# Kernel optimization log

Measured on AMD Instinct MI355X. Metric: run time of the kernel, lower is better.

## Reference

```python
import jax, jax.numpy as jnp
import numpy as np

D_MODEL = 512
D_STATE = 16
D_CONV = 4
EXPAND = 2
D_INNER = EXPAND * D_MODEL          # 1024
DT_RANK = (D_MODEL + 15) // 16      # 32
B, L = 32, 2048
EPS = 1e-12


def _ln(x, g, b):
    mu = jnp.mean(x, axis=-1, keepdims=True)
    var = jnp.mean(jnp.square(x - mu), axis=-1, keepdims=True)
    return (x - mu) * jax.lax.rsqrt(var + EPS) * g + b


def setup_inputs() -> dict:
    key = jax.random.key(0)
    ks = jax.random.split(key, 12)
    s = lambda fan: 1.0 / np.sqrt(fan)
    inp = {
        "input_tensor": jax.random.normal(ks[0], (B, L, D_MODEL), jnp.float32),
        # Mamba params
        "in_proj_w": jax.random.normal(ks[1], (2 * D_INNER, D_MODEL), jnp.float32) * s(D_MODEL),
        "conv_w": jax.random.normal(ks[2], (D_INNER, D_CONV), jnp.float32) * s(D_CONV),
        "conv_b": jnp.zeros((D_INNER,), jnp.float32),
        "x_proj_w": jax.random.normal(ks[3], (DT_RANK + 2 * D_STATE, D_INNER), jnp.float32) * s(D_INNER),
        "dt_proj_w": jax.random.normal(ks[4], (D_INNER, DT_RANK), jnp.float32) * s(DT_RANK),
        "dt_proj_b": jnp.full((D_INNER,), -4.0, jnp.float32),  # softplus(-4) ~ small dt
        "A_log": jnp.log(jnp.broadcast_to(jnp.arange(1, D_STATE + 1, dtype=jnp.float32), (D_INNER, D_STATE))),
        "D": jnp.ones((D_INNER,), jnp.float32),
        "out_proj_w": jax.random.normal(ks[5], (D_MODEL, D_INNER), jnp.float32) * s(D_INNER),
        # block params
        "ln1_g": jnp.ones((D_MODEL,), jnp.float32),
        "ln1_b": jnp.zeros((D_MODEL,), jnp.float32),
        "w1_w": jax.random.normal(ks[6], (4 * D_MODEL, D_MODEL), jnp.float32) * s(D_MODEL),
        "w1_b": jnp.zeros((4 * D_MODEL,), jnp.float32),
        "w2_w": jax.random.normal(ks[7], (D_MODEL, 4 * D_MODEL), jnp.float32) * s(4 * D_MODEL),
        "w2_b": jnp.zeros((D_MODEL,), jnp.float32),
        "ln2_g": jnp.ones((D_MODEL,), jnp.float32),
        "ln2_b": jnp.zeros((D_MODEL,), jnp.float32),
    }
    return inp


def _mamba(x, in_proj_w, conv_w, conv_b, x_proj_w, dt_proj_w, dt_proj_b, A_log, D, out_proj_w):
    # x: [B, L, d_model]
    xz = jnp.einsum("bld,ed->ble", x, in_proj_w)          # [B,L,2*d_inner]
    xi, z = jnp.split(xz, 2, axis=-1)                      # each [B,L,d_inner]

    # depthwise causal conv1d along L (d_conv taps)
    xpad = jnp.pad(xi, ((0, 0), (D_CONV - 1, 0), (0, 0)))
    conv = conv_b
    for k in range(D_CONV):
        conv = conv + xpad[:, k:k + L, :] * conv_w[:, k]
    u = jax.nn.silu(conv)                                  # [B,L,d_inner]

    # input-dependent dt, B, C
    x_dbl = jnp.einsum("bld,ed->ble", u, x_proj_w)         # [B,L,dt_rank+2N]
    dt, B_t, C_t = jnp.split(x_dbl, [DT_RANK, DT_RANK + D_STATE], axis=-1)
    delta = jax.nn.softplus(jnp.einsum("blr,dr->bld", dt, dt_proj_w) + dt_proj_b)  # [B,L,d_inner]

    A = -jnp.exp(A_log)                                    # [d_inner, N]

    def step(h, inp):
        u_t, d_t, Bt, Ct = inp                             # [B,d_in],[B,d_in],[B,N],[B,N]
        dA = jnp.exp(d_t[..., None] * A)                   # [B,d_in,N]
        h = h * dA + (d_t * u_t)[..., None] * Bt[:, None, :]
        y = jnp.sum(h * Ct[:, None, :], axis=-1)           # [B,d_in]
        return h, y

    h0 = jnp.zeros((B, D_INNER, D_STATE), u.dtype)
    xs = (jnp.swapaxes(u, 0, 1), jnp.swapaxes(delta, 0, 1),
          jnp.swapaxes(B_t, 0, 1), jnp.swapaxes(C_t, 0, 1))
    _, ys = jax.lax.scan(step, h0, xs)                     # [L,B,d_inner]
    y = jnp.swapaxes(ys, 0, 1) + u * D
    y = y * jax.nn.silu(z)
    return jnp.einsum("ble,de->bld", y, out_proj_w)        # [B,L,d_model]


def reference(input_tensor, in_proj_w, conv_w, conv_b, x_proj_w, dt_proj_w, dt_proj_b,
              A_log, D, out_proj_w, ln1_g, ln1_b, w1_w, w1_b, w2_w, w2_b, ln2_g, ln2_b):
    h = _mamba(input_tensor, in_proj_w, conv_w, conv_b, x_proj_w, dt_proj_w,
               dt_proj_b, A_log, D, out_proj_w)
    h = _ln(h + input_tensor, ln1_g, ln1_b)                # num_layers > 1 branch, dropout=0
    f = jax.nn.gelu(jnp.einsum("bld,fd->blf", h, w1_w) + w1_b, approximate=False)
    f = jnp.einsum("blf,df->bld", f, w2_w) + w2_b
    return _ln(f + h, ln2_g, ln2_b)
```

## Files before the change

kernel.cpp:

```cpp
#include <hip/hip_runtime.h>
#include <hip/hip_bf16.h>

#define DM 512
#define DI 1024
#define DC 4
#define DTR 32
#define NST 16
#define LSEQ 2048
#define NBATCH 32
#define NCH 16
#define CHL 128

typedef __attribute__((ext_vector_type(8))) short b16x8;
typedef __attribute__((ext_vector_type(4))) float fx4;
typedef __attribute__((ext_vector_type(4))) unsigned short u16x4;

__device__ __forceinline__ unsigned short f2bf(float f) {
    union { float f; unsigned u; } x; x.f = f;
    unsigned r = x.u + 0x7fffu + ((x.u >> 16) & 1u);
    return (unsigned short)(r >> 16);
}
__device__ __forceinline__ float bf2f(unsigned short u) {
    union { unsigned u; float f; } x; x.u = ((unsigned)u) << 16;
    return x.f;
}

__global__ __launch_bounds__(256) void cast_kernel(const float* __restrict__ src,
                                                   unsigned short* __restrict__ dst, int n4) {
    int i = blockIdx.x * 256 + threadIdx.x;
    if (i < n4) {
        fx4 v = *(const fx4*)&src[(size_t)i * 4];
        u16x4 o;
        #pragma unroll
        for (int j = 0; j < 4; j++) o[j] = f2bf(v[j]);
        *(u16x4*)&dst[(size_t)i * 4] = o;
    }
}

template <int BN, int BK, int EPI, bool HAS_BIAS>
__global__ __launch_bounds__(256, 3) void gemm_bf16(const unsigned short* __restrict__ A,
                                                    const unsigned short* __restrict__ W,
                                                    const float* __restrict__ bias,
                                                    void* __restrict__ Cout, int N, int K,
                                                    unsigned short* __restrict__ aux) {
    constexpr int BM = 128;
    constexpr int GPR = BK / 8;
    __shared__ __align__(16) unsigned short As[BM * BK];
    __shared__ __align__(16) unsigned short Ws[BN * BK];
    const int tid = threadIdx.x;
    const int wave = tid >> 6, lane = tid & 63;
    const int lr = lane & 15, lg = lane >> 4;
    const int ntx = gridDim.x;
    const int tot = ntx * gridDim.y;
    const int lin = blockIdx.y * ntx + blockIdx.x;
    const int cpx = tot >> 3;
    const int swz = (lin & 7) * cpx + (lin >> 3);
    const int m0 = (swz / ntx) * BM, n0 = (swz % ntx) * BN;
    const int wm0 = (wave >> 1) * 64, wn0 = (wave & 1) * (BN / 2);
    constexpr int NR = BN / 32;
    fx4 acc[4][NR];
    #pragma unroll
    for (int i = 0; i < 4; i++)
        #pragma unroll
        for (int j = 0; j < NR; j++) acc[i][j] = fx4{0.f, 0.f, 0.f, 0.f};

    for (int k0 = 0; k0 < K; k0 += BK) {
        #pragma unroll
        for (int i = 0; i < (BM * BK / 8) / 256; i++) {
            int cb = (i * 4 + wave) * 64, c = cb + lane;
            int row = c / GPR, kk = (c % GPR) * 8;
            const unsigned short* g = A + (size_t)(m0 + row) * K + k0 + kk;
            __builtin_amdgcn_global_load_lds(
                (const __attribute__((address_space(1))) unsigned int*)g,
                (__attribute__((address_space(3))) unsigned int*)&As[cb * 8], 16, 0, 0);
        }
        #pragma unroll
        for (int i = 0; i < (BN * BK / 8) / 256; i++) {
            int cb = (i * 4 + wave) * 64, c = cb + lane;
            int row = c / GPR, kk = (c % GPR) * 8;
            const unsigned short* g = W + (size_t)(n0 + row) * K + k0 + kk;
            __builtin_amdgcn_global_load_lds(
                (const __attribute__((address_space(1))) unsigned int*)g,
                (__attribute__((address_space(3))) unsigned int*)&Ws[cb * 8], 16, 0, 0);
        }
        __syncthreads();
        #pragma unroll
        for (int ks = 0; ks < BK / 32; ks++) {
            b16x8 af[4], bfr[NR];
            #pragma unroll
            for (int mi = 0; mi < 4; mi++)
                af[mi] = *(const b16x8*)&As[(wm0 + mi * 16 + lr) * BK + ks * 32 + lg * 8];
            #pragma unroll
            for (int ni = 0; ni < NR; ni++)
                bfr[ni] = *(const b16x8*)&Ws[(wn0 + ni * 16 + lr) * BK + ks * 32 + lg * 8];
            #pragma unroll
            for (int mi = 0; mi < 4; mi++)
                #pragma unroll
                for (int ni = 0; ni < NR; ni++)
                    acc[mi][ni] = __builtin_amdgcn_mfma_f32_16x16x32_bf16(af[mi], bfr[ni],
                                                                         acc[mi][ni], 0, 0, 0);
        }
        __syncthreads();
    }
    #pragma unroll
    for (int mi = 0; mi < 4; mi++) {
        #pragma unroll
        for (int ni = 0; ni < NR; ni++) {
            #pragma unroll
            for (int j2 = 0; j2 < 4; j2++) {
                int row = m0 + wm0 + mi * 16 + lg * 4 + j2;
                int col = n0 + wn0 + ni * 16 + lr;
                float v = acc[mi][ni][j2];
                if (HAS_BIAS) v += bias[col];
                size_t o = (size_t)row * N + col;
                if (EPI == 0) {
                    ((float*)Cout)[o] = v;
                } else if (EPI == 1) {
                    ((unsigned short*)Cout)[o] = f2bf(v);
                } else if (EPI == 2) {
                    v = 0.5f * v * (1.f + erff(v * 0.70710678118654752f));
                    ((unsigned short*)Cout)[o] = f2bf(v);
                } else if (EPI == 3) {
                    v = (v > 20.f) ? v : log1pf(__expf(v));
                    ((float*)Cout)[o] = v;
                } else if (EPI == 4) {
                    v = (v > 20.f) ? v : log1pf(__expf(v));
                    ((unsigned short*)Cout)[o] = f2bf(v);
                } else {
                    ((float*)Cout)[o] = v;
                    if (col < DTR) aux[(size_t)row * DTR + col] = f2bf(v);
                }
            }
        }
    }
}

__global__ __launch_bounds__(256) void conv_silu_kernel(const unsigned short* __restrict__ xz16,
                                                        const float* __restrict__ cw,
                                                        const float* __restrict__ cb,
                                                        unsigned short* __restrict__ u16) {
    int idx = blockIdx.x * 256 + threadIdx.x;
    int m = idx >> 7;
    int d0 = (idx & 127) << 3;
    int l = m & (LSEQ - 1);
    float acc[8];
    fx4 w0[8];
    #pragma unroll
    for (int j = 0; j < 8; j++) {
        acc[j] = cb[d0 + j];
        w0[j] = *(const fx4*)&cw[(d0 + j) * 4];
    }
    #pragma unroll
    for (int k = 0; k < 4; k++) {
        int lm = l - 3 + k;
        if (lm >= 0) {
            b16x8 xv = *(const b16x8*)&xz16[(size_t)(m - 3 + k) * (2 * DI) + d0];
            #pragma unroll
            for (int j = 0; j < 8; j++) acc[j] += bf2f((unsigned short)xv[j]) * w0[j][k];
        }
    }
    b16x8 o;
    #pragma unroll
    for (int j = 0; j < 8; j++) {
        float v = acc[j];
        v = v / (1.f + __expf(-v));
        o[j] = (short)f2bf(v);
    }
    *(b16x8*)&u16[(size_t)m * DI + d0] = o;
}

__device__ __forceinline__ bool load_A(const float* __restrict__ A_log, int d, float* Av) {
    bool fast = true;
    #pragma unroll
    for (int n = 0; n < NST; n++) {
        Av[n] = -__expf(A_log[(size_t)d * NST + n]);
        fast = fast && (fabsf(Av[n] + (float)(n + 1)) < 1e-4f * (float)(n + 1));
    }
    return fast;
}

__device__ __forceinline__ void en_tree(float e1, float* en) {
    float e2 = e1 * e1, e3 = e2 * e1, e4 = e2 * e2, e8 = e4 * e4, e12 = e8 * e4;
    en[0] = e1;        en[1] = e2;        en[2] = e3;        en[3] = e4;
    en[4] = e4 * e1;   en[5] = e4 * e2;   en[6] = e4 * e3;   en[7] = e8;
    en[8] = e8 * e1;   en[9] = e8 * e2;   en[10] = e8 * e3;  en[11] = e12;
    en[12] = e12 * e1; en[13] = e12 * e2; en[14] = e12 * e3; en[15] = e8 * e8;
}

__global__ __launch_bounds__(256) void scan_partial(const unsigned short* __restrict__ delta16,
                                                    const unsigned short* __restrict__ u16,
                                                    const float* __restrict__ xdbl,
                                                    const float* __restrict__ A_log,
                                                    float* __restrict__ sumd,
                                                    float* __restrict__ hend) {
    int d = blockIdx.x * 256 + threadIdx.x;
    int ch = blockIdx.y, b = blockIdx.z;
    size_t bL = (size_t)b * LSEQ + (size_t)ch * CHL;
    float Av[NST], h[NST];
    const bool fast = load_A(A_log, d, Av);
    #pragma unroll
    for (int n = 0; n < NST; n++) h[n] = 0.f;
    float S = 0.f;
    #pragma unroll 2
    for (int l = 0; l < CHL; l++) {
        size_t r = bL + l;
        float dl = bf2f(delta16[r * DI + d]);
        float uu = bf2f(u16[r * DI + d]);
        S += dl;
        float du = dl * uu;
        const float* xr = &xdbl[r * 64 + 32];
        float Bv[NST];
        #pragma unroll
        for (int t = 0; t < 4; t++) *(fx4*)&Bv[t * 4] = *(const fx4*)(xr + t * 4);
        float en[NST];
        if (fast) {
            en_tree(__expf(-dl), en);
        } else {
            #pragma unroll
            for (int n = 0; n < NST; n++) en[n] = __expf(dl * Av[n]);
        }
        #pragma unroll
        for (int n = 0; n < NST; n++) h[n] = h[n] * en[n] + du * Bv[n];
    }
    size_t base = ((size_t)(b * NCH + ch) * NST) * DI + d;
    #pragma unroll
    for (int n = 0; n < NST; n++) hend[base + (size_t)n * DI] = h[n];
    sumd[(size_t)(b * NCH + ch) * DI + d] = S;
}

__global__ __launch_bounds__(256) void scan_carry(const float* __restrict__ sumd,
                                                  const float* __restrict__ hend,
                                                  const float* __restrict__ A_log,
                                                  float* __restrict__ hin) {
    int d = blockIdx.x * 256 + threadIdx.x;
    int b = blockIdx.y;
    float Av[NST], h[NST];
    #pragma unroll
    for (int n = 0; n < NST; n++) {
        Av[n] = -__expf(A_log[(size_t)d * NST + n]);
        h[n] = 0.f;
    }
    for (int k = 0; k < NCH; k++) {
        size_t base = ((size_t)(b * NCH + k) * NST) * DI + d;
        #pragma unroll
        for (int n = 0; n < NST; n++) hin[base + (size_t)n * DI] = h[n];
        if (k < NCH - 1) {
            float S = sumd[(size_t)(b * NCH + k) * DI + d];
            #pragma unroll
            for (int n = 0; n < NST; n++)
                h[n] = h[n] * __expf(S * Av[n]) + hend[base + (size_t)n * DI];
        }
    }
}

__global__ __launch_bounds__(256) void scan_final(const unsigned short* __restrict__ delta16,
                                                  const unsigned short* u16,
                                                  const unsigned short* __restrict__ xz16,
                                                  const float* __restrict__ xdbl,
                                                  const float* __restrict__ A_log,
                                                  const float* __restrict__ Dp,
                                                  const float* __restrict__ hin,
                                                  unsigned short* y16) {
    int d = blockIdx.x * 256 + threadIdx.x;
    int ch = blockIdx.y, b = blockIdx.z;
    size_t bL = (size_t)b * LSEQ + (size_t)ch * CHL;
    float Av[NST], h[NST];
    const bool fast = load_A(A_log, d, Av);
    size_t base = ((size_t)(b * NCH + ch) * NST) * DI + d;
    #pragma unroll
    for (int n = 0; n < NST; n++) h[n] = hin[base + (size_t)n * DI];
    float Dd = Dp[d];
    #pragma unroll 2
    for (int l = 0; l < CHL; l++) {
        size_t r = bL + l;
        float dl = bf2f(delta16[r * DI + d]);
        float uu = bf2f(u16[r * DI + d]);
        float zz = bf2f(xz16[r * (2 * DI) + DI + d]);
        float du = dl * uu;
        const float* xr = &xdbl[r * 64 + 32];
        float Bv[NST], Cv[NST];
        #pragma unroll
        for (int t = 0; t < 4; t++) {
            *(fx4*)&Bv[t * 4] = *(const fx4*)(xr + t * 4);
            *(fx4*)&Cv[t * 4] = *(const fx4*)(xr + 16 + t * 4);
        }
        float en[NST];
        if (fast) {
            en_tree(__expf(-dl), en);
        } else {
            #pragma unroll
            for (int n = 0; n < NST; n++) en[n] = __expf(dl * Av[n]);
        }
        float y = 0.f;
        #pragma unroll
        for (int n = 0; n < NST; n++) {
            h[n] = h[n] * en[n] + du * Bv[n];
            y += h[n] * Cv[n];
        }
        y = (y + uu * Dd) * (zz / (1.f + __expf(-zz)));
        y16[r * DI + d] = f2bf(y);
    }
}

template <int AIN, int RIN, int OUT>
__global__ __launch_bounds__(256) void ln_kernel(const void* __restrict__ a,
                                                 const void* __restrict__ res,
                                                 const float* __restrict__ g,
                                                 const float* __restrict__ bta,
                                                 void* __restrict__ out) {
    int row = blockIdx.x, tid = threadIdx.x;
    size_t base = (size_t)row * DM;
    float a0, a1, r0, r1;
    if (AIN == 0) {
        a0 = ((const float*)a)[base + tid];
        a1 = ((const float*)a)[base + tid + 256];
    } else {
        a0 = bf2f(((const unsigned short*)a)[base + tid]);
        a1 = bf2f(((const unsigned short*)a)[base + tid + 256]);
    }
    if (RIN == 0) {
        r0 = ((const float*)res)[base + tid];
        r1 = ((const float*)res)[base + tid + 256];
    } else {
        r0 = bf2f(((const unsigned short*)res)[base + tid]);
        r1 = bf2f(((const unsigned short*)res)[base + tid + 256]);
    }
    float v0 = a0 + r0, v1 = a1 + r1;
    float s = v0 + v1, q = v0 * v0 + v1 * v1;
    #pragma unroll
    for (int m = 32; m >= 1; m >>= 1) {
        s += __shfl_xor(s, m);
        q += __shfl_xor(q, m);
    }
    __shared__ float rs[4], rq[4];
    int wv = tid >> 6;
    if ((tid & 63) == 0) { rs[wv] = s; rq[wv] = q; }
    __syncthreads();
    s = rs[0] + rs[1] + rs[2] + rs[3];
    q = rq[0] + rq[1] + rq[2] + rq[3];
    float mu = s * (1.f / DM);
    float var = q * (1.f / DM) - mu * mu;
    float rsg = rsqrtf(var + 1e-12f);
    float o0 = (v0 - mu) * rsg * g[tid] + bta[tid];
    float o1 = (v1 - mu) * rsg * g[tid + 256] + bta[tid + 256];
    if (OUT == 0) {
        ((float*)out)[base + tid] = o0;
        ((float*)out)[base + tid + 256] = o1;
    } else {
        ((unsigned short*)out)[base + tid] = f2bf(o0);
        ((unsigned short*)out)[base + tid + 256] = f2bf(o1);
    }
}

static size_t align256(size_t b) { return (b + 255) & ~(size_t)255; }

static size_t tier_need(size_t Gb) {
    size_t R = Gb * LSEQ;
    size_t w = 0;
    w += align256((size_t)2 * DI * DM * 2);
    w += align256((size_t)64 * DI * 2);
    w += align256((size_t)DM * DI * 2);
    w += align256((size_t)4 * DM * DM * 2);
    w += align256((size_t)DM * 4 * DM * 2);
    w += align256((size_t)DI * DTR * 2);
    w += align256(R * 2048 * 2);
    w += align256(R * 1024 * 2);
    w += align256(R * 1024 * 2);
    w += align256(R * 64 * 4);
    w += align256(R * 32 * 2);
    w += align256(R * 512 * 2);
    w += align256(Gb * NCH * DI * 4);
    w += align256(Gb * NCH * NST * DI * 4);
    w += align256(Gb * NCH * NST * DI * 4);
    return w;
}

extern "C" void kernel_launch(void* const* d_in, const int* in_sizes, int n_in,
                              void* d_out, int out_size, void* d_ws, size_t ws_size,
                              hipStream_t stream) {
    const float* x_in   = (const float*)d_in[0];
    const float* inpw   = (const float*)d_in[1];
    const float* convw  = (const float*)d_in[2];
    const float* convb  = (const float*)d_in[3];
    const float* xprojw = (const float*)d_in[4];
    const float* dtw    = (const float*)d_in[5];
    const float* dtb    = (const float*)d_in[6];
    const float* A_log  = (const float*)d_in[7];
    const float* Dp     = (const float*)d_in[8];
    const float* outpw  = (const float*)d_in[9];
    const float* ln1g   = (const float*)d_in[10];
    const float* ln1b   = (const float*)d_in[11];
    const float* w1w    = (const float*)d_in[12];
    const float* w1b    = (const float*)d_in[13];
    const float* w2w    = (const float*)d_in[14];
    const float* w2b    = (const float*)d_in[15];
    const float* ln2g   = (const float*)d_in[16];
    const float* ln2b   = (const float*)d_in[17];

    int G = 1;
    const int tiers[5] = {32, 16, 8, 4, 2};
    for (int t = 0; t < 5; t++) {
        if (ws_size >= tier_need((size_t)tiers[t])) { G = tiers[t]; break; }
    }
    const size_t R = (size_t)G * LSEQ;

    char* w = (char*)d_ws;
    auto alloc = [&](size_t bytes) { char* p = w; w += align256(bytes); return p; };

    unsigned short* win16 = (unsigned short*)alloc((size_t)2 * DI * DM * 2);
    unsigned short* wxp16 = (unsigned short*)alloc((size_t)64 * DI * 2);
    unsigned short* wop16 = (unsigned short*)alloc((size_t)DM * DI * 2);
    unsigned short* ww116 = (unsigned short*)alloc((size_t)4 * DM * DM * 2);
    unsigned short* ww216 = (unsigned short*)alloc((size_t)DM * 4 * DM * 2);
    unsigned short* wdt16 = (unsigned short*)alloc((size_t)DI * DTR * 2);
    unsigned short* xz16  = (unsigned short*)alloc(R * 2048 * 2);
    unsigned short* u16   = (unsigned short*)alloc(R * 1024 * 2);
    unsigned short* dreg  = (unsigned short*)alloc(R * 1024 * 2);
    float*          xdbl  = (float*)alloc(R * 64 * 4);
    unsigned short* dt16  = (unsigned short*)alloc(R * 32 * 2);
    unsigned short* x16   = (unsigned short*)alloc(R * 512 * 2);
    float*          sumd  = (float*)alloc((size_t)G * NCH * DI * 4);
    float*          hend  = (float*)alloc((size_t)G * NCH * NST * DI * 4);
    float*          hin   = (float*)alloc((size_t)G * NCH * NST * DI * 4);

    unsigned short* delta16 = dreg;
    unsigned short* y16 = u16;
    unsigned short* f16 = xz16;
    unsigned short* mm16 = dreg;
    unsigned short* w2o16 = dreg;
    unsigned short* h16  = x16;

    dim3 blk(256);
    cast_kernel<<<(2 * DI * DM / 4 + 255) / 256, blk, 0, stream>>>(inpw, win16, 2 * DI * DM / 4);
    cast_kernel<<<(64 * DI / 4 + 255) / 256, blk, 0, stream>>>(xprojw, wxp16, 64 * DI / 4);
    cast_kernel<<<(DM * DI / 4 + 255) / 256, blk, 0, stream>>>(outpw, wop16, DM * DI / 4);
    cast_kernel<<<(4 * DM * DM / 4 + 255) / 256, blk, 0, stream>>>(w1w, ww116, 4 * DM * DM / 4);
    cast_kernel<<<(DM * 4 * DM / 4 + 255) / 256, blk, 0, stream>>>(w2w, ww216, DM * 4 * DM / 4);
    cast_kernel<<<(DI * DTR / 4 + 255) / 256, blk, 0, stream>>>(dtw, wdt16, DI * DTR / 4);

    for (int grp = 0; grp < NBATCH / G; grp++) {
        const size_t rb = (size_t)grp * R;
        const float* xg = x_in + rb * DM;
        cast_kernel<<<(int)(R * DM / 4 / 256), blk, 0, stream>>>(xg, x16, (int)(R * DM / 4));
        gemm_bf16<128, 64, 1, false><<<dim3(2 * DI / 128, R / 128), blk, 0, stream>>>(
            x16, win16, nullptr, xz16, 2 * DI, DM, nullptr);
        conv_silu_kernel<<<(int)(R * (DI / 8) / 256), blk, 0, stream>>>(xz16, convw, convb, u16);
        gemm_bf16<64, 64, 5, false><<<dim3(1, R / 128), blk, 0, stream>>>(
            u16, wxp16, nullptr, xdbl, 64, DI, dt16);
        gemm_bf16<128, 32, 4, true><<<dim3(DI / 128, R / 128), blk, 0, stream>>>(
            dt16, wdt16, dtb, delta16, DI, DTR, nullptr);
        scan_partial<<<dim3(DI / 256, NCH - 1, G), blk, 0, stream>>>(
            delta16, u16, xdbl, A_log, sumd, hend);
        scan_carry<<<dim3(DI / 256, G), blk, 0, stream>>>(sumd, hend, A_log, hin);
        scan_final<<<dim3(DI / 256, NCH, G), blk, 0, stream>>>(
            delta16, u16, xz16, xdbl, A_log, Dp, hin, y16);
        gemm_bf16<128, 64, 1, false><<<dim3(DM / 128, R / 128), blk, 0, stream>>>(
            y16, wop16, nullptr, mm16, DM, DI, nullptr);
        ln_kernel<1, 0, 1><<<(int)R, blk, 0, stream>>>(mm16, xg, ln1g, ln1b, h16);
        gemm_bf16<128, 64, 2, true><<<dim3(4 * DM / 128, R / 128), blk, 0, stream>>>(
            h16, ww116, w1b, f16, 4 * DM, DM, nullptr);
        gemm_bf16<128, 64, 1, true><<<dim3(DM / 128, R / 128), blk, 0, stream>>>(
            f16, ww216, w2b, w2o16, DM, 4 * DM, nullptr);
        ln_kernel<1, 1, 0><<<(int)R, blk, 0, stream>>>(w2o16, h16, ln2g, ln2b,
                                                       (float*)d_out + rb * DM);
    }
}
```

Baseline: 1.736 ms.

## Shorten scan chunks, reuse conv window, one-wave layernorm rows, merge carry buffer

The chunked selective scan now uses 32 chunks of 64 steps instead of 16 of 128, which doubles parallelism in the partial and final scan kernels but lengthens the serial carry pass. The depthwise conv kernel now processes 8 consecutive timesteps per thread with a sliding register window, so each input row is loaded once instead of four times. Layernorm assigns one wavefront per row with vectorized 8-element loads and drops the shared-memory reduction and barrier. The carry kernel writes carried states back into the hend buffer in place, removing the separate hin allocation and its traffic.

```diff
diff --git a/kernel.cpp b/kernel.cpp
--- a/kernel.cpp
+++ b/kernel.cpp
@@ -8,8 +8,8 @@
 #define NST 16
 #define LSEQ 2048
 #define NBATCH 32
-#define NCH 16
-#define CHL 128
+#define NCH 32
+#define CHL 64
 
 typedef __attribute__((ext_vector_type(8))) short b16x8;
 typedef __attribute__((ext_vector_type(4))) float fx4;
@@ -140,33 +140,52 @@
                                                         const float* __restrict__ cb,
                                                         unsigned short* __restrict__ u16) {
     int idx = blockIdx.x * 256 + threadIdx.x;
-    int m = idx >> 7;
+    int strip = idx >> 7;
     int d0 = (idx & 127) << 3;
-    int l = m & (LSEQ - 1);
-    float acc[8];
+    int m0 = strip * 8;
+    int l0 = m0 & (LSEQ - 1);
     fx4 w0[8];
+    float bias[8];
     #pragma unroll
     for (int j = 0; j < 8; j++) {
-        acc[j] = cb[d0 + j];
+        bias[j] = cb[d0 + j];
         w0[j] = *(const fx4*)&cw[(d0 + j) * 4];
     }
-    #pragma unroll
-    for (int k = 0; k < 4; k++) {
-        int lm = l - 3 + k;
+    float win[3][8];
+    #pragma unroll
+    for (int t = 0; t < 3; t++) {
+        int lm = l0 - 3 + t;
         if (lm >= 0) {
-            b16x8 xv = *(const b16x8*)&xz16[(size_t)(m - 3 + k) * (2 * DI) + d0];
-            #pragma unroll
-            for (int j = 0; j < 8; j++) acc[j] += bf2f((unsigned short)xv[j]) * w0[j][k];
-        }
-    }
-    b16x8 o;
+            b16x8 xv = *(const b16x8*)&xz16[(size_t)(m0 - 3 + t) * (2 * DI) + d0];
+            #pragma unroll
+            for (int i = 0; i < 8; i++) win[t][i] = bf2f((unsigned short)xv[i]);
+        } else {
+            #pragma unroll
+            for (int i = 0; i < 8; i++) win[t][i] = 0.f;
+        }
+    }
     #pragma unroll
     for (int j = 0; j < 8; j++) {
-        float v = acc[j];
-        v = v / (1.f + __expf(-v));
-        o[j] = (short)f2bf(v);
-    }
-    *(b16x8*)&u16[(size_t)m * DI + d0] = o;
+        float cur[8];
+        b16x8 xv = *(const b16x8*)&xz16[(size_t)(m0 + j) * (2 * DI) + d0];
+        #pragma unroll
+        for (int i = 0; i < 8; i++) cur[i] = bf2f((unsigned short)xv[i]);
+        b16x8 o;
+        #pragma unroll
+        for (int i = 0; i < 8; i++) {
+            float v = bias[i] + win[0][i] * w0[i][0] + win[1][i] * w0[i][1] +
+                      win[2][i] * w0[i][2] + cur[i] * w0[i][3];
+            v = v / (1.f + __expf(-v));
+            o[i] = (short)f2bf(v);
+        }
+        *(b16x8*)&u16[(size_t)(m0 + j) * DI + d0] = o;
+        #pragma unroll
+        for (int i = 0; i < 8; i++) {
+            win[0][i] = win[1][i];
+            win[1][i] = win[2][i];
+            win[2][i] = cur[i];
+        }
+    }
 }
 
 __device__ __forceinline__ bool load_A(const float* __restrict__ A_log, int d, float* Av) {
@@ -229,9 +248,8 @@
 }
 
 __global__ __launch_bounds__(256) void scan_carry(const float* __restrict__ sumd,
-                                                  const float* __restrict__ hend,
-                                                  const float* __restrict__ A_log,
-                                                  float* __restrict__ hin) {
+                                                  float* __restrict__ hend,
+                                                  const float* __restrict__ A_log) {
     int d = blockIdx.x * 256 + threadIdx.x;
     int b = blockIdx.y;
     float Av[NST], h[NST];
@@ -242,13 +260,18 @@
     }
     for (int k = 0; k < NCH; k++) {
         size_t base = ((size_t)(b * NCH + k) * NST) * DI + d;
-        #pragma unroll
-        for (int n = 0; n < NST; n++) hin[base + (size_t)n * DI] = h[n];
         if (k < NCH - 1) {
             float S = sumd[(size_t)(b * NCH + k) * DI + d];
-            #pragma unroll
-            for (int n = 0; n < NST; n++)
-                h[n] = h[n] * __expf(S * Av[n]) + hend[base + (size_t)n * DI];
+            float he[NST];
+            #pragma unroll
+            for (int n = 0; n < NST; n++) he[n] = hend[base + (size_t)n * DI];
+            #pragma unroll
+            for (int n = 0; n < NST; n++) hend[base + (size_t)n * DI] = h[n];
+            #pragma unroll
+            for (int n = 0; n < NST; n++) h[n] = h[n] * __expf(S * Av[n]) + he[n];
+        } else {
+            #pragma unroll
+            for (int n = 0; n < NST; n++) hend[base + (size_t)n * DI] = h[n];
         }
     }
 }
@@ -308,47 +331,60 @@
                                                  const float* __restrict__ g,
                                                  const float* __restrict__ bta,
                                                  void* __restrict__ out) {
-    int row = blockIdx.x, tid = threadIdx.x;
+    int lane = threadIdx.x & 63;
+    int row = blockIdx.x * 4 + (threadIdx.x >> 6);
     size_t base = (size_t)row * DM;
-    float a0, a1, r0, r1;
+    int c0 = lane * 8;
+    float av[8], rv[8];
     if (AIN == 0) {
-        a0 = ((const float*)a)[base + tid];
-        a1 = ((const float*)a)[base + tid + 256];
+        *(fx4*)&av[0] = *(const fx4*)&((const float*)a)[base + c0];
+        *(fx4*)&av[4] = *(const fx4*)&((const float*)a)[base + c0 + 4];
     } else {
-        a0 = bf2f(((const unsigned short*)a)[base + tid]);
-        a1 = bf2f(((const unsigned short*)a)[base + tid + 256]);
+        b16x8 t = *(const b16x8*)&((const unsigned short*)a)[base + c0];
+        #pragma unroll
+        for (int i = 0; i < 8; i++) av[i] = bf2f((unsigned short)t[i]);
     }
     if (RIN == 0) {
-        r0 = ((const float*)res)[base + tid];
-        r1 = ((const float*)res)[base + tid + 256];
+        *(fx4*)&rv[0] = *(const fx4*)&((const float*)res)[base + c0];
+        *(fx4*)&rv[4] = *(const fx4*)&((const float*)res)[base + c0 + 4];
     } else {
-        r0 = bf2f(((const unsigned short*)res)[base + tid]);
-        r1 = bf2f(((const unsigned short*)res)[base + tid + 256]);
-    }
-    float v0 = a0 + r0, v1 = a1 + r1;
-    float s = v0 + v1, q = v0 * v0 + v1 * v1;
+        b16x8 t = *(const b16x8*)&((const unsigned short*)res)[base + c0];
+        #pragma unroll
+        for (int i = 0; i < 8; i++) rv[i] = bf2f((unsigned short)t[i]);
+    }
+    float v[8], s = 0.f, q = 0.f;
+    #pragma unroll
+    for (int i = 0; i < 8; i++) {
+        v[i] = av[i] + rv[i];
+        s += v[i];
+        q += v[i] * v[i];
+    }
     #pragma unroll
     for (int m = 32; m >= 1; m >>= 1) {
         s += __shfl_xor(s, m);
         q += __shfl_xor(q, m);
     }
-    __shared__ float rs[4], rq[4];
-    int wv = tid >> 6;
-    if ((tid & 63) == 0) { rs[wv] = s; rq[wv] = q; }
-    __syncthreads();
-    s = rs[0] + rs[1] + rs[2] + rs[3];
-    q = rq[0] + rq[1] + rq[2] + rq[3];
     float mu = s * (1.f / DM);
     float var = q * (1.f / DM) - mu * mu;
     float rsg = rsqrtf(var + 1e-12f);
-    float o0 = (v0 - mu) * rsg * g[tid] + bta[tid];
-    float o1 = (v1 - mu) * rsg * g[tid + 256] + bta[tid + 256];
+    float gv[8], bv[8];
+    *(fx4*)&gv[0] = *(const fx4*)&g[c0];
+    *(fx4*)&gv[4] = *(const fx4*)&g[c0 + 4];
+    *(fx4*)&bv[0] = *(const fx4*)&bta[c0];
+    *(fx4*)&bv[4] = *(const fx4*)&bta[c0 + 4];
     if (OUT == 0) {
-        ((float*)out)[base + tid] = o0;
-        ((float*)out)[base + tid + 256] = o1;
+        fx4 o0, o1;
+        #pragma unroll
+        for (int i = 0; i < 4; i++) o0[i] = (v[i] - mu) * rsg * gv[i] + bv[i];
+        #pragma unroll
+        for (int i = 0; i < 4; i++) o1[i] = (v[4 + i] - mu) * rsg * gv[4 + i] + bv[4 + i];
+        *(fx4*)&((float*)out)[base + c0] = o0;
+        *(fx4*)&((float*)out)[base + c0 + 4] = o1;
     } else {
-        ((unsigned short*)out)[base + tid] = f2bf(o0);
-        ((unsigned short*)out)[base + tid + 256] = f2bf(o1);
+        b16x8 o;
+        #pragma unroll
+        for (int i = 0; i < 8; i++) o[i] = (short)f2bf((v[i] - mu) * rsg * gv[i] + bv[i]);
+        *(b16x8*)&((unsigned short*)out)[base + c0] = o;
     }
 }
 
@@ -370,7 +406,6 @@
     w += align256(R * 32 * 2);
     w += align256(R * 512 * 2);
     w += align256(Gb * NCH * DI * 4);
-    w += align256(Gb * NCH * NST * DI * 4);
     w += align256(Gb * NCH * NST * DI * 4);
     return w;
 }
@@ -421,7 +456,6 @@
     unsigned short* x16   = (unsigned short*)alloc(R * 512 * 2);
     float*          sumd  = (float*)alloc((size_t)G * NCH * DI * 4);
     float*          hend  = (float*)alloc((size_t)G * NCH * NST * DI * 4);
-    float*          hin   = (float*)alloc((size_t)G * NCH * NST * DI * 4);
 
     unsigned short* delta16 = dreg;
     unsigned short* y16 = u16;
@@ -444,24 +478,24 @@
         cast_kernel<<<(int)(R * DM / 4 / 256), blk, 0, stream>>>(xg, x16, (int)(R * DM / 4));
         gemm_bf16<128, 64, 1, false><<<dim3(2 * DI / 128, R / 128), blk, 0, stream>>>(
             x16, win16, nullptr, xz16, 2 * DI, DM, nullptr);
-        conv_silu_kernel<<<(int)(R * (DI / 8) / 256), blk, 0, stream>>>(xz16, convw, convb, u16);
+        conv_silu_kernel<<<(int)(R / 16), blk, 0, stream>>>(xz16, convw, convb, u16);
         gemm_bf16<64, 64, 5, false><<<dim3(1, R / 128), blk, 0, stream>>>(
             u16, wxp16, nullptr, xdbl, 64, DI, dt16);
         gemm_bf16<128, 32, 4, true><<<dim3(DI / 128, R / 128), blk, 0, stream>>>(
             dt16, wdt16, dtb, delta16, DI, DTR, nullptr);
         scan_partial<<<dim3(DI / 256, NCH - 1, G), blk, 0, stream>>>(
             delta16, u16, xdbl, A_log, sumd, hend);
-        scan_carry<<<dim3(DI / 256, G), blk, 0, stream>>>(sumd, hend, A_log, hin);
+        scan_carry<<<dim3(DI / 256, G), blk, 0, stream>>>(sumd, hend, A_log);
         scan_final<<<dim3(DI / 256, NCH, G), blk, 0, stream>>>(
-            delta16, u16, xz16, xdbl, A_log, Dp, hin, y16);
+            delta16, u16, xz16, xdbl, A_log, Dp, hend, y16);
         gemm_bf16<128, 64, 1, false><<<dim3(DM / 128, R / 128), blk, 0, stream>>>(
             y16, wop16, nullptr, mm16, DM, DI, nullptr);
-        ln_kernel<1, 0, 1><<<(int)R, blk, 0, stream>>>(mm16, xg, ln1g, ln1b, h16);
+        ln_kernel<1, 0, 1><<<(int)(R / 4), blk, 0, stream>>>(mm16, xg, ln1g, ln1b, h16);
         gemm_bf16<128, 64, 2, true><<<dim3(4 * DM / 128, R / 128), blk, 0, stream>>>(
             h16, ww116, w1b, f16, 4 * DM, DM, nullptr);
         gemm_bf16<128, 64, 1, true><<<dim3(DM / 128, R / 128), blk, 0, stream>>>(
             f16, ww216, w2b, w2o16, DM, 4 * DM, nullptr);
-        ln_kernel<1, 1, 0><<<(int)R, blk, 0, stream>>>(w2o16, h16, ln2g, ln2b,
-                                                       (float*)d_out + rb * DM);
-    }
-}
+        ln_kernel<1, 1, 0><<<(int)(R / 4), blk, 0, stream>>>(w2o16, h16, ln2g, ln2b,
+                                                             (float*)d_out + rb * DM);
+    }
+}
```

After: 1.639 ms. 5.6% less time.
